# Performance work log

Measured on AMD Instinct MI355X. Metric: run time of the kernel, lower is better.

Reference implementation:

```python
import jax, jax.numpy as jnp
import numpy as np

BN_EPS = 1e-5


def _posit_intervals():
    # Replicates conditions_l1 / conditions_g1 interval tables (128 steps each).
    l1, g1 = [], []
    for e in range(16):
        for j in range(8):
            if j == 0:
                l1.append((0.0, 1.0625 / 2**16, 1.0 / 2**16))
            else:
                lo = (1.0625 + 0.125 * (j - 1)) / 2 ** (16 - e)
                hi = (1.0625 + 0.125 * j) / 2 ** (16 - e)
                l1.append((lo, hi, 0.5 * (lo + hi)))
            lo = (1.0625 + 0.125 * (j - 1)) * 2 ** e
            hi = (1.0625 + 0.125 * j) * 2 ** e
            g1.append((lo, hi, 0.5 * (lo + hi)))  # note: j==8 branch in torch code is dead
    return l1, g1

_L1, _G1 = _posit_intervals()


def posit_quantize(x):
    # Faithful emulation of the 128 sequential torch.where passes.
    ax = jnp.abs(x)          # conditions are fixed from the ORIGINAL tensor
    neg = x < 0
    y = x
    for (lo1, hi1, m1), (log_, hig, mg) in zip(_L1, _G1):
        c1 = jnp.logical_and(ax > lo1, ax < hi1)
        cg = jnp.logical_and(ax > log_, ax < hig)
        v1 = jnp.where(neg, -m1, m1).astype(x.dtype)
        vg = jnp.where(neg, -mg, mg).astype(x.dtype)
        # |y| < 1 gate uses the CURRENT tensor, as in the torch loop
        y = jnp.where(jnp.abs(y) < 1, jnp.where(c1, v1, y), jnp.where(cg, vg, y))
    return y


def conv1x1(x, w, b):
    # x: [N,C,D,H,W], w: [O,C] (kernel_size=1), b: [O]
    return jnp.einsum('ncdhw,oc->nodhw', x, w) + b[None, :, None, None, None]


def batchnorm(x, gamma, beta, mean, var):
    inv = gamma / jnp.sqrt(var + BN_EPS)
    return x * inv[None, :, None, None, None] + (beta - mean * inv)[None, :, None, None, None]


def setup_inputs() -> dict:
    key = jax.random.key(0)
    ks = jax.random.split(key, 12)
    C = 256
    x = jax.random.normal(ks[0], (8, C, 16, 32, 32), dtype=jnp.float32)
    w1 = jax.random.normal(ks[1], (C, C), dtype=jnp.float32) * 0.05
    b1 = jax.random.normal(ks[2], (C,), dtype=jnp.float32) * 0.05
    w2 = jax.random.normal(ks[3], (C, C), dtype=jnp.float32) * 0.05
    b2 = jax.random.normal(ks[4], (C,), dtype=jnp.float32) * 0.05
    g1 = jax.random.uniform(ks[5], (C,)) + 0.5
    be1 = jax.random.normal(ks[6], (C,)) * 0.1
    m1 = jax.random.normal(ks[7], (C,)) * 0.1
    v1 = jax.random.uniform(ks[8], (C,)) + 0.5
    g2 = jax.random.uniform(ks[9], (C,)) + 0.5
    be2 = jax.random.normal(ks[10], (C,)) * 0.1
    m2 = jax.random.normal(ks[11], (C,)) * 0.1
    v2 = jax.random.uniform(jax.random.fold_in(key, 99), (C,)) + 0.5
    return {"x": x, "w1": w1, "b1": b1, "g1": g1, "be1": be1, "m1": m1, "v1": v1,
            "w2": w2, "b2": b2, "g2": g2, "be2": be2, "m2": m2, "v2": v2}


def reference(x, w1, b1, g1, be1, m1, v1, w2, b2, g2, be2, m2, v2):
    residual = x
    out = conv1x1(posit_quantize(x), posit_quantize(w1), b1)
    out = jax.nn.relu(batchnorm(out, g1, be1, m1, v1))
    out = conv1x1(posit_quantize(out), posit_quantize(w2), b2)
    out = batchnorm(out, g2, be2, m2, v2)
    return jax.nn.relu(out + residual)
```

## Files before the change

### kernel.cpp

```cpp
#include <hip/hip_runtime.h>

typedef __attribute__((ext_vector_type(8))) short short8;
typedef __attribute__((ext_vector_type(4))) short s4v;
typedef __attribute__((ext_vector_type(4))) float floatx4;

#define SPOS 16384

__device__ __forceinline__ unsigned short f2bf(float f) {
    unsigned u = __float_as_uint(f);
    u += 0x7fffu + ((u >> 16) & 1u);
    return (unsigned short)(u >> 16);
}

__device__ __forceinline__ float posit_q(float x) {
    unsigned xu  = __float_as_uint(x);
    unsigned sgn = xu & 0x80000000u;
    unsigned au  = xu & 0x7fffffffu;
    unsigned m   = au & 0x007fffffu;
    unsigned r   = (au + 0x00080000u) & 0xfff00000u;
    bool bdry = (m & 0x000fffffu) == 0x00080000u;
    unsigned res;
    if (au >= 0x3f800000u) {
        res = r;
        if (m > 0x00700000u && m < 0x00780000u && au < 0x47700000u)
            res = (au & 0xff800000u) + 0x00800000u;
        if ((bdry && m != 0x00780000u) || au >= 0x47780000u)
            res = au;
    } else {
        res = (m <= 0x00080000u || m >= 0x00780000u || bdry) ? au : r;
        if (au < 0x37880000u) res = au ? 0x37800000u : 0u;
    }
    return __uint_as_float(sgn | res);
}

__device__ __forceinline__ float posit_q_pos(float z) {
    unsigned au  = __float_as_uint(z);
    unsigned m   = au & 0x007fffffu;
    unsigned r   = (au + 0x00080000u) & 0xfff00000u;
    bool bdry = (m & 0x000fffffu) == 0x00080000u;
    unsigned res;
    if (au >= 0x3f800000u) {
        res = r;
        if (m > 0x00700000u && m < 0x00780000u && au < 0x47700000u)
            res = (au & 0xff800000u) + 0x00800000u;
        if ((bdry && m != 0x00780000u) || au >= 0x47780000u)
            res = au;
    } else {
        res = (m <= 0x00080000u || m >= 0x00780000u || bdry) ? au : r;
        if (au < 0x37880000u) res = au ? 0x37800000u : 0u;
    }
    return __uint_as_float(res);
}

__global__ __launch_bounds__(256) void prep_kernel(
    const float* __restrict__ w1, const float* __restrict__ w2,
    const float* __restrict__ b1, const float* __restrict__ g1,
    const float* __restrict__ be1, const float* __restrict__ m1,
    const float* __restrict__ v1,
    const float* __restrict__ b2, const float* __restrict__ g2,
    const float* __restrict__ be2, const float* __restrict__ m2,
    const float* __restrict__ v2,
    unsigned short* __restrict__ w1p, unsigned short* __restrict__ w2p,
    float* __restrict__ cst)
{
    int i = blockIdx.x * 256 + threadIdx.x;
    if (i < 65536) {
        const int j    = i & 7;
        const int lane = (i >> 3) & 63;
        const int kb   = (i >> 9) & 7;
        const int G    = i >> 12;
        const int row  = 16 * G + (lane & 15);
        const int k    = 32 * kb + 8 * (lane >> 4) + j;
        w1p[i] = f2bf(posit_q(w1[row * 256 + k]));
        w2p[i] = f2bf(posit_q(w2[row * 256 + k]));
        if (i < 256) {
            float inv1 = g1[i] / sqrtf(v1[i] + 1e-5f);
            cst[i]       = inv1;
            cst[256 + i] = fmaf(b1[i], inv1, be1[i] - m1[i] * inv1);
            float inv2 = g2[i] / sqrtf(v2[i] + 1e-5f);
            cst[512 + i] = inv2;
            cst[768 + i] = fmaf(b2[i], inv2, be2[i] - m2[i] * inv2);
        }
    }
}

__device__ __forceinline__ int qidx(int p, int cb) {
    return p * 256 + ((cb ^ (p & 31)) << 3);
}

__global__ __launch_bounds__(256, 3) void fused_kernel(
    const float* __restrict__ x,
    const unsigned short* __restrict__ w1p,
    const unsigned short* __restrict__ w2p,
    const float* __restrict__ cst,
    float* __restrict__ out)
{
    __shared__ alignas(16) unsigned short q[64 * 256];
    __shared__ alignas(16) float xs[4 * 1024];

    const int b  = blockIdx.x;
    const int n  = b >> 8;
    const int s0 = (b & 255) << 6;
    const float* xb = x   + (size_t)n * (256 * SPOS) + s0;
    float*       ob = out + (size_t)n * (256 * SPOS) + s0;

    const int t    = threadIdx.x;
    const int lane = t & 63;
    const int w    = t >> 6;
    const int quad = lane >> 4;
    const int l15  = lane & 15;

    {
        const int g  = lane & 15;
        const int co = lane >> 4;
        float* xsw = xs + w * 1024;
        const float* src0 = xb + (size_t)(64 * w + co) * SPOS + 4 * g;
        floatx4 v[16];
        #pragma unroll
        for (int r = 0; r < 8; ++r) {
            v[2 * r]     = *(const floatx4*)(src0 + (size_t)(8 * r) * SPOS);
            v[2 * r + 1] = *(const floatx4*)(src0 + (size_t)(8 * r + 4) * SPOS);
        }
        #pragma unroll
        for (int r = 0; r < 8; ++r) {
            float* xr = xsw + (r & 1) * 512;
            *(floatx4*)&xr[co * 64 + ((4 * g) ^ (4 * co))]             = v[2 * r];
            *(floatx4*)&xr[(co + 4) * 64 + ((4 * g) ^ (4 * (co + 4)))] = v[2 * r + 1];
            short8 pk;
            #pragma unroll
            for (int c8 = 0; c8 < 8; ++c8)
                pk[c8] = (short)f2bf(posit_q(xr[c8 * 64 + (lane ^ (4 * c8))]));
            *(short8*)&q[qidx(lane, 8 * w + r)] = pk;
        }
    }
    __syncthreads();

    floatx4 acc[4][4];
    #pragma unroll
    for (int i = 0; i < 4; ++i)
        #pragma unroll
        for (int jj = 0; jj < 4; ++jj)
            acc[i][jj] = (floatx4)0.0f;

    #pragma unroll
    for (int kk = 0; kk < 256; kk += 32) {
        short8 af[4], bf[4];
        #pragma unroll
        for (int i = 0; i < 4; ++i)
            af[i] = *(const short8*)&w1p[(((w * 4 + i) * 8 + (kk >> 5)) * 64 + lane) * 8];
        #pragma unroll
        for (int jj = 0; jj < 4; ++jj)
            bf[jj] = *(const short8*)&q[qidx(16 * jj + l15, (kk >> 3) + quad)];
        #pragma unroll
        for (int i = 0; i < 4; ++i)
            #pragma unroll
            for (int jj = 0; jj < 4; ++jj)
                acc[i][jj] = __builtin_amdgcn_mfma_f32_16x16x32_bf16(af[i], bf[jj], acc[i][jj], 0, 0, 0);
    }

    short8 af20[4];
    #pragma unroll
    for (int i = 0; i < 4; ++i)
        af20[i] = *(const short8*)&w2p[(((w * 4 + i) * 8 + 0) * 64 + lane) * 8];

    __syncthreads();

    const int mbase = w * 64;

    {
        const float* sc1 = cst;
        const float* bi1 = cst + 256;
        #pragma unroll
        for (int i = 0; i < 4; ++i) {
            const int m0 = mbase + 16 * i + quad * 4;
            float sc[4], bi[4];
            #pragma unroll
            for (int r = 0; r < 4; ++r) { sc[r] = sc1[m0 + r]; bi[r] = bi1[m0 + r]; }
            #pragma unroll
            for (int jj = 0; jj < 4; ++jj) {
                const int p = 16 * jj + l15;
                s4v h;
                #pragma unroll
                for (int r = 0; r < 4; ++r) {
                    float z = fmaf(acc[i][jj][r], sc[r], bi[r]);
                    z = fmaxf(z, 0.0f);
                    h[r] = (short)f2bf(posit_q_pos(z));
                }
                *(s4v*)&q[qidx(p, m0 >> 3) + (m0 & 7)] = h;
            }
        }
    }
    __syncthreads();

    #pragma unroll
    for (int i = 0; i < 4; ++i)
        #pragma unroll
        for (int jj = 0; jj < 4; ++jj)
            acc[i][jj] = (floatx4)0.0f;

    #pragma unroll
    for (int kk = 0; kk < 256; kk += 32) {
        short8 af[4], bf[4];
        #pragma unroll
        for (int i = 0; i < 4; ++i)
            af[i] = (kk == 0) ? af20[i]
                  : *(const short8*)&w2p[(((w * 4 + i) * 8 + (kk >> 5)) * 64 + lane) * 8];
        #pragma unroll
        for (int jj = 0; jj < 4; ++jj)
            bf[jj] = *(const short8*)&q[qidx(16 * jj + l15, (kk >> 3) + quad)];
        #pragma unroll
        for (int i = 0; i < 4; ++i)
            #pragma unroll
            for (int jj = 0; jj < 4; ++jj)
                acc[i][jj] = __builtin_amdgcn_mfma_f32_16x16x32_bf16(bf[jj], af[i], acc[i][jj], 0, 0, 0);
    }

    __syncthreads();

    {
        const float* sc2 = cst + 512;
        const float* bi2 = cst + 768;
        float* stg = (float*)q + w * 2048;
        #pragma unroll
        for (int h = 0; h < 2; ++h) {
            #pragma unroll
            for (int i2 = 0; i2 < 2; ++i2) {
                const int chl = 16 * i2 + l15;
                #pragma unroll
                for (int jj = 0; jj < 4; ++jj)
                    *(floatx4*)&stg[chl * 64 + 4 * ((4 * jj + quad) ^ l15)] = acc[2 * h + i2][jj];
            }
            #pragma unroll
            for (int k = 0; k < 8; ++k) {
                const int chl = 4 * k + quad;
                const int ch  = mbase + 32 * h + chl;
                const size_t off = (size_t)ch * SPOS + 4 * l15;
                floatx4 v   = *(const floatx4*)&stg[chl * 64 + 4 * (l15 ^ (chl & 15))];
                floatx4 res = *(const floatx4*)(xb + off);
                const float sc = sc2[ch];
                const float bi = bi2[ch];
                floatx4 o;
                #pragma unroll
                for (int r = 0; r < 4; ++r)
                    o[r] = fmaxf(fmaf(v[r], sc, bi) + res[r], 0.0f);
                *(floatx4*)(ob + off) = o;
            }
        }
    }
}

extern "C" void kernel_launch(void* const* d_in, const int* in_sizes, int n_in,
                              void* d_out, int out_size, void* d_ws, size_t ws_size,
                              hipStream_t stream) {
    const float* x   = (const float*)d_in[0];
    const float* w1  = (const float*)d_in[1];
    const float* b1  = (const float*)d_in[2];
    const float* g1  = (const float*)d_in[3];
    const float* be1 = (const float*)d_in[4];
    const float* m1  = (const float*)d_in[5];
    const float* v1  = (const float*)d_in[6];
    const float* w2  = (const float*)d_in[7];
    const float* b2  = (const float*)d_in[8];
    const float* g2  = (const float*)d_in[9];
    const float* be2 = (const float*)d_in[10];
    const float* m2  = (const float*)d_in[11];
    const float* v2  = (const float*)d_in[12];

    unsigned short* w1p = (unsigned short*)d_ws;
    unsigned short* w2p = w1p + 65536;
    float* cst = (float*)(w2p + 65536);

    prep_kernel<<<256, 256, 0, stream>>>(w1, w2, b1, g1, be1, m1, v1,
                                         b2, g2, be2, m2, v2, w1p, w2p, cst);
    fused_kernel<<<2048, 256, 0, stream>>>(x, w1p, w2p, cst, (float*)d_out);
}
```

Baseline: 327.5 us.

## Halve spatial tile to 32 positions per block and raise occupancy

Each block now handles 32 spatial positions instead of 64, doubling the grid to 4096 blocks. LDS use and accumulator registers are halved, and the launch bound is raised to 4 blocks per CU. The LDS swizzles are reworked to match the new tile shape, and the residual loads in the epilogue are hoisted so they are issued before the staging writes. The aim is more waves in flight to hide memory latency. In exchange, each fetched weight fragment feeds half as many MFMAs, so weight reuse per block drops, and global rows are read in 128-byte pieces instead of 256-byte pieces.

```diff
diff --git a/kernel.cpp b/kernel.cpp
--- a/kernel.cpp
+++ b/kernel.cpp
@@ -88,19 +88,19 @@
     return p * 256 + ((cb ^ (p & 31)) << 3);
 }
 
-__global__ __launch_bounds__(256, 3) void fused_kernel(
+__global__ __launch_bounds__(256, 4) void fused_kernel(
     const float* __restrict__ x,
     const unsigned short* __restrict__ w1p,
     const unsigned short* __restrict__ w2p,
     const float* __restrict__ cst,
     float* __restrict__ out)
 {
-    __shared__ alignas(16) unsigned short q[64 * 256];
-    __shared__ alignas(16) float xs[4 * 1024];
+    __shared__ alignas(16) unsigned short q[32 * 256];
+    __shared__ alignas(16) float xs[4 * 512];
 
     const int b  = blockIdx.x;
-    const int n  = b >> 8;
-    const int s0 = (b & 255) << 6;
+    const int n  = b >> 9;
+    const int s0 = (b & 511) << 5;
     const float* xb = x   + (size_t)n * (256 * SPOS) + s0;
     float*       ob = out + (size_t)n * (256 * SPOS) + s0;
 
@@ -111,50 +111,51 @@
     const int l15  = lane & 15;
 
     {
-        const int g  = lane & 15;
-        const int co = lane >> 4;
-        float* xsw = xs + w * 1024;
+        const int g  = lane & 7;
+        const int co = lane >> 3;
+        float* xsw = xs + w * 512;
         const float* src0 = xb + (size_t)(64 * w + co) * SPOS + 4 * g;
-        floatx4 v[16];
-        #pragma unroll
-        for (int r = 0; r < 8; ++r) {
-            v[2 * r]     = *(const floatx4*)(src0 + (size_t)(8 * r) * SPOS);
-            v[2 * r + 1] = *(const floatx4*)(src0 + (size_t)(8 * r + 4) * SPOS);
-        }
-        #pragma unroll
-        for (int r = 0; r < 8; ++r) {
-            float* xr = xsw + (r & 1) * 512;
-            *(floatx4*)&xr[co * 64 + ((4 * g) ^ (4 * co))]             = v[2 * r];
-            *(floatx4*)&xr[(co + 4) * 64 + ((4 * g) ^ (4 * (co + 4)))] = v[2 * r + 1];
+        floatx4 v[8];
+        #pragma unroll
+        for (int r = 0; r < 8; ++r)
+            v[r] = *(const floatx4*)(src0 + (size_t)(8 * r) * SPOS);
+        const int p5 = lane & 31, half = lane >> 5;
+        #pragma unroll
+        for (int dr = 0; dr < 4; ++dr) {
+            *(floatx4*)&xsw[co * 32 + 4 * (g ^ co)]       = v[2 * dr];
+            *(floatx4*)&xsw[(co + 8) * 32 + 4 * (g ^ co)] = v[2 * dr + 1];
             short8 pk;
             #pragma unroll
-            for (int c8 = 0; c8 < 8; ++c8)
-                pk[c8] = (short)f2bf(posit_q(xr[c8 * 64 + (lane ^ (4 * c8))]));
-            *(short8*)&q[qidx(lane, 8 * w + r)] = pk;
-        }
-    }
-    __syncthreads();
-
-    floatx4 acc[4][4];
+            for (int j = 0; j < 8; ++j) {
+                const int cl = 8 * half + j;
+                const float val = xsw[cl * 32 + 4 * ((p5 >> 2) ^ (cl & 7)) + (p5 & 3)];
+                pk[j] = (short)f2bf(posit_q(val));
+            }
+            *(short8*)&q[qidx(p5, 8 * w + 2 * dr + half)] = pk;
+        }
+    }
+    __syncthreads();
+
+    floatx4 acc[4][2];
     #pragma unroll
     for (int i = 0; i < 4; ++i)
         #pragma unroll
-        for (int jj = 0; jj < 4; ++jj)
+        for (int jj = 0; jj < 2; ++jj)
             acc[i][jj] = (floatx4)0.0f;
 
     #pragma unroll
-    for (int kk = 0; kk < 256; kk += 32) {
-        short8 af[4], bf[4];
-        #pragma unroll
-        for (int i = 0; i < 4; ++i)
-            af[i] = *(const short8*)&w1p[(((w * 4 + i) * 8 + (kk >> 5)) * 64 + lane) * 8];
-        #pragma unroll
-        for (int jj = 0; jj < 4; ++jj)
-            bf[jj] = *(const short8*)&q[qidx(16 * jj + l15, (kk >> 3) + quad)];
-        #pragma unroll
-        for (int i = 0; i < 4; ++i)
-            #pragma unroll
-            for (int jj = 0; jj < 4; ++jj)
+    for (int kk = 0; kk < 8; ++kk) {
+        short8 af[4], bf[2];
+        #pragma unroll
+        for (int i = 0; i < 4; ++i)
+            af[i] = *(const short8*)&w1p[(((w * 4 + i) * 8 + kk) * 64 + lane) * 8];
+        #pragma unroll
+        for (int jj = 0; jj < 2; ++jj)
+            bf[jj] = *(const short8*)&q[qidx(16 * jj + l15, 4 * kk + quad)];
+        #pragma unroll
+        for (int i = 0; i < 4; ++i)
+            #pragma unroll
+            for (int jj = 0; jj < 2; ++jj)
                 acc[i][jj] = __builtin_amdgcn_mfma_f32_16x16x32_bf16(af[i], bf[jj], acc[i][jj], 0, 0, 0);
     }
 
@@ -177,7 +178,7 @@
             #pragma unroll
             for (int r = 0; r < 4; ++r) { sc[r] = sc1[m0 + r]; bi[r] = bi1[m0 + r]; }
             #pragma unroll
-            for (int jj = 0; jj < 4; ++jj) {
+            for (int jj = 0; jj < 2; ++jj) {
                 const int p = 16 * jj + l15;
                 s4v h;
                 #pragma unroll
@@ -195,23 +196,23 @@
     #pragma unroll
     for (int i = 0; i < 4; ++i)
         #pragma unroll
-        for (int jj = 0; jj < 4; ++jj)
+        for (int jj = 0; jj < 2; ++jj)
             acc[i][jj] = (floatx4)0.0f;
 
     #pragma unroll
-    for (int kk = 0; kk < 256; kk += 32) {
-        short8 af[4], bf[4];
+    for (int kk = 0; kk < 8; ++kk) {
+        short8 af[4], bf[2];
         #pragma unroll
         for (int i = 0; i < 4; ++i)
             af[i] = (kk == 0) ? af20[i]
-                  : *(const short8*)&w2p[(((w * 4 + i) * 8 + (kk >> 5)) * 64 + lane) * 8];
-        #pragma unroll
-        for (int jj = 0; jj < 4; ++jj)
-            bf[jj] = *(const short8*)&q[qidx(16 * jj + l15, (kk >> 3) + quad)];
-        #pragma unroll
-        for (int i = 0; i < 4; ++i)
-            #pragma unroll
-            for (int jj = 0; jj < 4; ++jj)
+                  : *(const short8*)&w2p[(((w * 4 + i) * 8 + kk) * 64 + lane) * 8];
+        #pragma unroll
+        for (int jj = 0; jj < 2; ++jj)
+            bf[jj] = *(const short8*)&q[qidx(16 * jj + l15, 4 * kk + quad)];
+        #pragma unroll
+        for (int i = 0; i < 4; ++i)
+            #pragma unroll
+            for (int jj = 0; jj < 2; ++jj)
                 acc[i][jj] = __builtin_amdgcn_mfma_f32_16x16x32_bf16(bf[jj], af[i], acc[i][jj], 0, 0, 0);
     }
 
@@ -220,30 +221,39 @@
     {
         const float* sc2 = cst + 512;
         const float* bi2 = cst + 768;
-        float* stg = (float*)q + w * 2048;
+        float* stg = (float*)q + w * 1024;
+        const int row_g = lane >> 3, g = lane & 7;
+
+        floatx4 res[2][4];
+        #pragma unroll
+        for (int h = 0; h < 2; ++h)
+            #pragma unroll
+            for (int k = 0; k < 4; ++k) {
+                const int ch = mbase + 32 * h + 8 * k + row_g;
+                res[h][k] = *(const floatx4*)(xb + (size_t)ch * SPOS + 4 * g);
+            }
+
         #pragma unroll
         for (int h = 0; h < 2; ++h) {
             #pragma unroll
             for (int i2 = 0; i2 < 2; ++i2) {
                 const int chl = 16 * i2 + l15;
                 #pragma unroll
-                for (int jj = 0; jj < 4; ++jj)
-                    *(floatx4*)&stg[chl * 64 + 4 * ((4 * jj + quad) ^ l15)] = acc[2 * h + i2][jj];
-            }
-            #pragma unroll
-            for (int k = 0; k < 8; ++k) {
-                const int chl = 4 * k + quad;
+                for (int jj = 0; jj < 2; ++jj)
+                    *(floatx4*)&stg[chl * 32 + 4 * ((4 * jj + quad) ^ (chl & 7))] = acc[2 * h + i2][jj];
+            }
+            #pragma unroll
+            for (int k = 0; k < 4; ++k) {
+                const int chl = 8 * k + row_g;
                 const int ch  = mbase + 32 * h + chl;
-                const size_t off = (size_t)ch * SPOS + 4 * l15;
-                floatx4 v   = *(const floatx4*)&stg[chl * 64 + 4 * (l15 ^ (chl & 15))];
-                floatx4 res = *(const floatx4*)(xb + off);
+                floatx4 v = *(const floatx4*)&stg[chl * 32 + 4 * (g ^ row_g)];
                 const float sc = sc2[ch];
                 const float bi = bi2[ch];
                 floatx4 o;
                 #pragma unroll
                 for (int r = 0; r < 4; ++r)
-                    o[r] = fmaxf(fmaf(v[r], sc, bi) + res[r], 0.0f);
-                *(floatx4*)(ob + off) = o;
+                    o[r] = fmaxf(fmaf(v[r], sc, bi) + res[h][k][r], 0.0f);
+                *(floatx4*)(ob + (size_t)ch * SPOS + 4 * g) = o;
             }
         }
     }
@@ -272,5 +282,5 @@
 
     prep_kernel<<<256, 256, 0, stream>>>(w1, w2, b1, g1, be1, m1, v1,
                                          b2, g2, be2, m2, v2, w1p, w2p, cst);
-    fused_kernel<<<2048, 256, 0, stream>>>(x, w1p, w2p, cst, (float*)d_out);
-}
+    fused_kernel<<<4096, 256, 0, stream>>>(x, w1p, w2p, cst, (float*)d_out);
+}
```

New measurement: 325.6 us. Within noise of the previous version (-0.6%).
